# Optimization experiments

Measured on AMD Instinct MI355X. Metric: run time of the kernel, lower is better.

Reference implementation:

```python
import jax, jax.numpy as jnp
import numpy as np

B, L, C = 4, 8192, 256
HEADS = 1
DP = C // HEADS
FFN_HID = C * 2 * 4  # (d_model*2) * ffn_dim_expansion
EPS = 1e-5


def _layernorm(x, gamma, beta):
    mu = jnp.mean(x, axis=-1, keepdims=True)
    var = jnp.var(x, axis=-1, keepdims=True)
    return (x - mu) * jax.lax.rsqrt(var + EPS) * gamma + beta


def setup_inputs() -> dict:
    key = jax.random.key(0)
    ks = jax.random.split(key, 12)
    s = 0.02
    return {
        "source": jax.random.normal(ks[0], (B, L, C), jnp.float32),
        "target": jax.random.normal(ks[1], (B, L, C), jnp.float32),
        "Wq": jax.random.normal(ks[2], (C, C), jnp.float32) * s,
        "Wk": jax.random.normal(ks[3], (C, C), jnp.float32) * s,
        "Wv": jax.random.normal(ks[4], (C, C), jnp.float32) * s,
        "Wl": jax.random.normal(ks[5], (C, C), jnp.float32) * s,
        "gamma1": jnp.ones((C,), jnp.float32),
        "beta1": jnp.zeros((C,), jnp.float32),
        "W1": jax.random.normal(ks[6], (2 * C, FFN_HID), jnp.float32) * s,
        "b1": jnp.zeros((FFN_HID,), jnp.float32),
        "W2": jax.random.normal(ks[7], (FFN_HID, C), jnp.float32) * s,
        "b2": jnp.zeros((C,), jnp.float32),
        "gamma2": jnp.ones((C,), jnp.float32),
        "beta2": jnp.zeros((C,), jnp.float32),
        "h": 64,
        "w": 128,
    }


def reference(source, target, Wq, Wk, Wv, Wl, gamma1, beta1, W1, b1, W2, b2,
              gamma2, beta2, h, w):
    assert L == h * w
    q = (source @ Wq).reshape(B, L, HEADS, DP)
    k = (target @ Wk).reshape(B, L, HEADS, DP)
    v = (target @ Wv).reshape(B, L, HEADS, DP)
    k = jax.nn.softmax(k, axis=1)  # softmax over token dim
    context = jnp.einsum('bnhd,bnhe->bhde', q, k)   # small d×d per head
    attn = jnp.einsum('bhde,bnhe->bnhd', context, v).reshape(B, L, C)
    message = _layernorm(attn @ Wl, gamma1, beta1)
    hidden = jax.nn.gelu(jnp.concatenate([source, message], axis=-1) @ W1 + b1,
                         approximate=False)
    message = _layernorm(hidden @ W2 + b2, gamma2, beta2)
    return source + message
```

## Files before the change

### kernel.cpp

```cpp
#include <hip/hip_runtime.h>
#include <hip/hip_bf16.h>

typedef unsigned short u16;
typedef __attribute__((ext_vector_type(8))) short short8;
typedef __attribute__((ext_vector_type(4))) float f32x4;

#define B_    4
#define L_    8192
#define C_    256
#define BL_   (B_*L_)
#define BLC_  (BL_*C_)
#define FFN_  2048
#define KCAT_ 512
#define EPS_  1e-5f

__device__ __forceinline__ float bf2f(u16 v) {
  union { unsigned int u; float f; } x; x.u = ((unsigned int)v) << 16; return x.f;
}
__device__ __forceinline__ u16 f2bf(float f) {
  union { float f; unsigned int u; } x; x.f = f;
  unsigned int lsb = (x.u >> 16) & 1u;
  return (u16)((x.u + 0x7fffu + lsb) >> 16);
}
__device__ __forceinline__ float gelu_f(float x) {
  float z = fabsf(x) * 0.70710678118654752f;
  float t = __builtin_amdgcn_rcpf(1.f + 0.3275911f * z);
  float p = ((((1.061405429f * t - 1.453152027f) * t + 1.421413741f) * t
              - 0.284496736f) * t + 0.254829592f) * t;
  float e = __expf(-z * z);
  float erfv = copysignf(1.f - p * e, x);
  return 0.5f * x * (1.f + erfv);
}

template<int MODE, int ACT, int SPLITK>
__launch_bounds__(256, 2)
__global__ void gemm_abt(const u16* __restrict__ A0, const u16* __restrict__ A1,
                         int SEL, int lda,
                         const u16* __restrict__ Bt,
                         const float* __restrict__ bias,
                         u16* __restrict__ Cb, float* __restrict__ Cf,
                         int M, int N, int K,
                         long sAb, long sBb, long sCb)
{
  __shared__ __align__(16) u16 As[2 * 128 * 32];
  __shared__ __align__(16) u16 Bs[2 * 128 * 32];

  const int ntiles = N >> 7;
  const int tile = blockIdx.x;
  const int mt0 = (tile / ntiles) << 7;
  const int nt0 = (tile % ntiles) << 7;
  const int kchunk = K / (int)gridDim.y;
  const int k0beg = blockIdx.y * kchunk;
  const int k0end = k0beg + kchunk;
  const int bz = blockIdx.z;
  A0 += (long)bz * sAb;  A1 += (long)bz * sAb;  Bt += (long)bz * sBb;

  const u16* Abase = (MODE == 2 && nt0 >= SEL) ? A1 : A0;

  const int tid  = threadIdx.x;
  const int wave = tid >> 6, lane = tid & 63;
  const int srow = lane >> 2;
  const int cq   = lane & 3;
  const int gq   = cq ^ (srow & 3);
  const int frow = lane & 15;
  const int fq   = lane >> 4;
  const int fqx  = (fq ^ (frow & 3)) * 8;

  f32x4 zero = {0.f, 0.f, 0.f, 0.f};
  f32x4 acc[4][4];
#pragma unroll
  for (int i = 0; i < 4; i++)
#pragma unroll
    for (int j = 0; j < 4; j++) acc[i][j] = zero;

  const int wm = (wave & 1) * 64, wn = (wave >> 1) * 64;

  for (int k0 = k0beg; k0 < k0end; k0 += 64) {
    __syncthreads();
    const u16* Asrc;
    int ka;
    if (MODE == 1) {
      const bool lo = (k0 < SEL);
      Asrc = lo ? A0 : A1;
      ka = lo ? k0 : (k0 - SEL);
    } else { Asrc = Abase; ka = k0; }

#pragma unroll
    for (int h = 0; h < 2; h++) {
#pragma unroll
      for (int i = 0; i < 2; i++) {
        const int chunk = i * 4 + wave;
        const u16* ga = Asrc + (long)(mt0 + chunk * 16 + srow) * lda
                        + (ka + h * 32 + gq * 8);
        __builtin_amdgcn_global_load_lds(
            (const __attribute__((address_space(1))) unsigned int*)ga,
            (__attribute__((address_space(3))) unsigned int*)&As[h * 4096 + chunk * 16 * 32],
            16, 0, 0);
        const u16* gb = Bt + (long)(nt0 + chunk * 16 + srow) * K
                        + (k0 + h * 32 + gq * 8);
        __builtin_amdgcn_global_load_lds(
            (const __attribute__((address_space(1))) unsigned int*)gb,
            (__attribute__((address_space(3))) unsigned int*)&Bs[h * 4096 + chunk * 16 * 32],
            16, 0, 0);
      }
    }
    __syncthreads();

#pragma unroll
    for (int h = 0; h < 2; h++) {
      short8 af[4], bf[4];
#pragma unroll
      for (int t = 0; t < 4; t++)
        af[t] = *(const short8*)&As[h * 4096 + (wm + t * 16 + frow) * 32 + fqx];
#pragma unroll
      for (int t = 0; t < 4; t++)
        bf[t] = *(const short8*)&Bs[h * 4096 + (wn + t * 16 + frow) * 32 + fqx];
#pragma unroll
      for (int mt = 0; mt < 4; mt++)
#pragma unroll
        for (int nt = 0; nt < 4; nt++)
          acc[mt][nt] = __builtin_amdgcn_mfma_f32_16x16x32_bf16(af[mt], bf[nt], acc[mt][nt], 0, 0, 0);
    }
  }

  if (SPLITK) {
    float* Cp = Cf + (long)bz * sCb;
#pragma unroll
    for (int mt = 0; mt < 4; mt++)
#pragma unroll
      for (int r = 0; r < 4; r++) {
        const int row = mt0 + wm + mt * 16 + fq * 4 + r;
#pragma unroll
        for (int nt = 0; nt < 4; nt++) {
          const int col = nt0 + wn + nt * 16 + frow;
          atomicAdd(&Cp[(long)row * N + col], acc[mt][nt][r]);
        }
      }
  } else {
    u16* Cp = Cb + (long)bz * sCb;
    float bv[4];
#pragma unroll
    for (int nt = 0; nt < 4; nt++)
      bv[nt] = bias ? bias[nt0 + wn + nt * 16 + frow] : 0.f;
#pragma unroll
    for (int mt = 0; mt < 4; mt++)
#pragma unroll
      for (int r = 0; r < 4; r++) {
        const int row = mt0 + wm + mt * 16 + fq * 4 + r;
#pragma unroll
        for (int nt = 0; nt < 4; nt++) {
          const int col = nt0 + wn + nt * 16 + frow;
          float v = acc[mt][nt][r] + bv[nt];
          if (ACT == 1) v = gelu_f(v);
          Cp[(long)row * N + col] = f2bf(v);
        }
      }
  }
}

__global__ void transpose2d(const u16* __restrict__ in, u16* __restrict__ out,
                            int R, int Cc, int ldi, long sIb, long sOb)
{
  __shared__ u16 t[32][33];
  const int bx = blockIdx.x * 32;
  const int by = blockIdx.y * 32;
  in  += (long)blockIdx.z * sIb;
  out += (long)blockIdx.z * sOb;
  const int tx = threadIdx.x, ty = threadIdx.y;
#pragma unroll
  for (int i = ty; i < 32; i += 8)
    t[i][tx] = in[(long)(by + i) * ldi + bx + tx];
  __syncthreads();
#pragma unroll
  for (int i = ty; i < 32; i += 8)
    out[(long)(bx + i) * R + by + tx] = t[tx][i];
}

__global__ void transpose_f2b(const float* __restrict__ in, u16* __restrict__ out,
                              int R, int Cc)
{
  __shared__ u16 t[32][33];
  const int bx = blockIdx.x * 32;
  const int by = blockIdx.y * 32;
  const int tx = threadIdx.x, ty = threadIdx.y;
#pragma unroll
  for (int i = ty; i < 32; i += 8)
    t[i][tx] = f2bf(in[(long)(by + i) * Cc + bx + tx]);
  __syncthreads();
#pragma unroll
  for (int i = ty; i < 32; i += 8)
    out[(long)(bx + i) * R + by + tx] = t[tx][i];
}

__global__ void pack_w256(const float* __restrict__ w0, const float* __restrict__ w1,
                          const float* __restrict__ w2, const float* __restrict__ w3,
                          u16* __restrict__ qkvT, u16* __restrict__ wlT)
{
  __shared__ u16 t[32][33];
  const int z = blockIdx.z;
  const float* in = (z == 0) ? w0 : (z == 1) ? w1 : (z == 2) ? w2 : w3;
  u16* out = (z < 3) ? (qkvT + (long)z * C_ * C_) : wlT;
  const int bx = blockIdx.x * 32, by = blockIdx.y * 32;
  const int tx = threadIdx.x, ty = threadIdx.y;
#pragma unroll
  for (int i = ty; i < 32; i += 8)
    t[i][tx] = f2bf(in[(long)(by + i) * C_ + bx + tx]);
  __syncthreads();
#pragma unroll
  for (int i = ty; i < 32; i += 8)
    out[(long)(bx + i) * C_ + by + tx] = t[tx][i];
}

__global__ void cast2_f2b(const float* __restrict__ in0, const float* __restrict__ in1,
                          u16* __restrict__ out0, u16* __restrict__ out1)
{
  const float* in = blockIdx.y ? in1 : in0;
  u16* out = blockIdx.y ? out1 : out0;
  int i = (blockIdx.x * 256 + threadIdx.x) * 4;
  float4 v = *(const float4*)(in + i);
  ushort4 o; o.x = f2bf(v.x); o.y = f2bf(v.y); o.z = f2bf(v.z); o.w = f2bf(v.w);
  *(ushort4*)(out + i) = o;
}

__global__ void softmax_rows(u16* __restrict__ data, int rowlen)
{
  const long base = (long)blockIdx.x * rowlen;
  const int tid = threadIdx.x, wave = tid >> 6, lane = tid & 63;
  __shared__ float red[4];

  float m = -3.4e38f;
  for (int i = tid; i < rowlen; i += 256) m = fmaxf(m, bf2f(data[base + i]));
#pragma unroll
  for (int off = 32; off; off >>= 1) m = fmaxf(m, __shfl_xor(m, off, 64));
  if (lane == 0) red[wave] = m;
  __syncthreads();
  m = fmaxf(fmaxf(red[0], red[1]), fmaxf(red[2], red[3]));
  __syncthreads();

  float s = 0.f;
  for (int i = tid; i < rowlen; i += 256) s += expf(bf2f(data[base + i]) - m);
#pragma unroll
  for (int off = 32; off; off >>= 1) s += __shfl_xor(s, off, 64);
  if (lane == 0) red[wave] = s;
  __syncthreads();
  const float inv = 1.f / (red[0] + red[1] + red[2] + red[3]);
  for (int i = tid; i < rowlen; i += 256)
    data[base + i] = f2bf(expf(bf2f(data[base + i]) - m) * inv);
}

template<int OUTF>
__global__ void layernorm_rows(const u16* __restrict__ x,
                               const float* __restrict__ gamma,
                               const float* __restrict__ beta,
                               const float* __restrict__ src,
                               void* __restrict__ outv)
{
  const int wave = threadIdx.x >> 6, lane = threadIdx.x & 63;
  const long row = (long)blockIdx.x * 4 + wave;
  ushort4 raw = ((const ushort4*)(x + row * C_))[lane];
  float v0 = bf2f(raw.x), v1 = bf2f(raw.y), v2 = bf2f(raw.z), v3 = bf2f(raw.w);
  float s = v0 + v1 + v2 + v3;
  float q = v0 * v0 + v1 * v1 + v2 * v2 + v3 * v3;
#pragma unroll
  for (int off = 32; off; off >>= 1) {
    s += __shfl_xor(s, off, 64);
    q += __shfl_xor(q, off, 64);
  }
  const float mu  = s * (1.f / C_);
  const float var = q * (1.f / C_) - mu * mu;
  const float rs  = 1.f / sqrtf(var + EPS_);
  float4 gr = ((const float4*)gamma)[lane];
  float4 br = ((const float4*)beta)[lane];
  float o0 = (v0 - mu) * rs * gr.x + br.x;
  float o1 = (v1 - mu) * rs * gr.y + br.y;
  float o2 = (v2 - mu) * rs * gr.z + br.z;
  float o3 = (v3 - mu) * rs * gr.w + br.w;
  if (OUTF) {
    float4 sr = ((const float4*)(src + row * C_))[lane];
    float4 ow; ow.x = o0 + sr.x; ow.y = o1 + sr.y; ow.z = o2 + sr.z; ow.w = o3 + sr.w;
    ((float4*)((float*)outv + row * C_))[lane] = ow;
  } else {
    ushort4 ow; ow.x = f2bf(o0); ow.y = f2bf(o1); ow.z = f2bf(o2); ow.w = f2bf(o3);
    ((ushort4*)((u16*)outv + row * C_))[lane] = ow;
  }
}

__global__ void zero_f32(float* __restrict__ p, int n) {
  int i = blockIdx.x * 256 + threadIdx.x;
  if (i < n) p[i] = 0.f;
}
__global__ void f32_to_bf16_k(const float* __restrict__ in, u16* __restrict__ out, int n) {
  int i = blockIdx.x * 256 + threadIdx.x;
  if (i < n) out[i] = f2bf(in[i]);
}

extern "C" void kernel_launch(void* const* d_in, const int* in_sizes, int n_in,
                              void* d_out, int out_size, void* d_ws, size_t ws_size,
                              hipStream_t stream)
{
  const float* source = (const float*)d_in[0];
  const float* target = (const float*)d_in[1];
  const float* Wq     = (const float*)d_in[2];
  const float* Wk     = (const float*)d_in[3];
  const float* Wv     = (const float*)d_in[4];
  const float* Wl     = (const float*)d_in[5];
  const float* gamma1 = (const float*)d_in[6];
  const float* beta1  = (const float*)d_in[7];
  const float* W1     = (const float*)d_in[8];
  const float* b1     = (const float*)d_in[9];
  const float* W2     = (const float*)d_in[10];
  const float* b2     = (const float*)d_in[11];
  const float* gamma2 = (const float*)d_in[12];
  const float* beta2  = (const float*)d_in[13];
  (void)in_sizes; (void)n_in; (void)out_size;

  char* ws = (char*)d_ws;
  size_t off = 0;
  auto take = [&](size_t bytes) -> char* {
    char* p = ws + off; off += (bytes + 255) & ~(size_t)255; return p;
  };
  u16*   WqkvT = (u16*)take((size_t)768 * C_ * 2);
  u16*   WlT   = (u16*)take((size_t)C_ * C_ * 2);
  u16*   W1T   = (u16*)take((size_t)FFN_ * KCAT_ * 2);
  u16*   W2T   = (u16*)take((size_t)C_ * FFN_ * 2);
  float* ctxTf = (float*)take((size_t)B_ * C_ * C_ * 4);
  u16*   ctxTb = (u16*)take((size_t)B_ * C_ * C_ * 2);
  u16*   Mtb   = (u16*)take((size_t)B_ * C_ * C_ * 2);
  u16*   srcB  = (u16*)take((size_t)BLC_ * 2);
  u16*   bufB  = (u16*)take((size_t)BLC_ * 2);
  u16*   bufD  = (u16*)take((size_t)BLC_ * 2);
  u16*   bufE  = (u16*)take((size_t)BLC_ * 2);
  const size_t ubase = off;
  u16* tgtB = (u16*)(ws + ubase);
  u16* QKV  = (u16*)(ws + ubase + (size_t)BLC_ * 2);
  u16* qT   = (u16*)(ws + ubase + (size_t)BLC_ * 2 + (size_t)BL_ * 768 * 2);
  u16* kT   = qT + (size_t)BLC_;
  const size_t live = (size_t)BLC_ * 2 * 3 + (size_t)BL_ * 768 * 2;
  int nchunk = 1;
  while (nchunk < 16) {
    size_t hid = (size_t)(BL_ / nchunk) * FFN_ * 2;
    size_t need = ubase + (hid > live ? hid : live);
    if (need <= ws_size) break;
    nchunk <<= 1;
  }
  const int Mc = BL_ / nchunk;
  u16* hidden = (u16*)(ws + ubase);

  dim3 tb(32, 8);
  cast2_f2b<<<dim3(BLC_ / 1024, 2), 256, 0, stream>>>(source, target, srcB, tgtB);
  pack_w256<<<dim3(8, 8, 4), tb, 0, stream>>>(Wq, Wk, Wv, Wl, WqkvT, WlT);
  transpose_f2b<<<dim3(FFN_/32, KCAT_/32), tb, 0, stream>>>(W1, W1T, KCAT_, FFN_);
  transpose_f2b<<<dim3(C_/32,  FFN_/32), tb, 0, stream>>>(W2, W2T, FFN_, C_);
  zero_f32<<<(B_*C_*C_)/256, 256, 0, stream>>>(ctxTf, B_*C_*C_);

  gemm_abt<2,0,0><<<dim3((BL_/128)*(768/128)), 256, 0, stream>>>(
      srcB, tgtB, 256, C_, WqkvT, nullptr, QKV, nullptr, BL_, 768, C_, 0, 0, 0);

  transpose2d<<<dim3(C_/32, L_/32, B_), tb, 0, stream>>>(QKV,       qT, L_, C_, 768, (long)L_*768, (long)L_*C_);
  transpose2d<<<dim3(C_/32, L_/32, B_), tb, 0, stream>>>(QKV + 256, kT, L_, C_, 768, (long)L_*768, (long)L_*C_);
  softmax_rows<<<B_*C_, 256, 0, stream>>>(kT, L_);

  gemm_abt<0,0,1><<<dim3(4, 16, B_), 256, 0, stream>>>(
      kT, kT, 0, L_, qT, nullptr, nullptr, ctxTf, C_, C_, L_,
      (long)C_*L_, (long)C_*L_, (long)C_*C_);
  f32_to_bf16_k<<<(B_*C_*C_)/256, 256, 0, stream>>>(ctxTf, ctxTb, B_*C_*C_);

  gemm_abt<0,0,0><<<dim3(4, 1, B_), 256, 0, stream>>>(
      WlT, WlT, 0, C_, ctxTb, nullptr, Mtb, nullptr, C_, C_, C_,
      0, (long)C_*C_, (long)C_*C_);

  gemm_abt<0,0,0><<<dim3((L_/128)*(C_/128), 1, B_), 256, 0, stream>>>(
      QKV + 512, QKV + 512, 0, 768, Mtb, nullptr, bufB, nullptr, L_, C_, C_,
      (long)L_*768, (long)C_*C_, (long)L_*C_);

  layernorm_rows<0><<<BL_/4, 256, 0, stream>>>(bufB, gamma1, beta1, nullptr, bufD);

  for (int ch = 0; ch < nchunk; ch++) {
    const long moff = (long)ch * Mc;
    gemm_abt<1,1,0><<<dim3((Mc/128)*(FFN_/128)), 256, 0, stream>>>(
        srcB + moff * C_, bufD + moff * C_, C_, C_, W1T, b1, hidden, nullptr,
        Mc, FFN_, KCAT_, 0, 0, 0);
    gemm_abt<0,0,0><<<dim3((Mc/128)*(C_/128)), 256, 0, stream>>>(
        hidden, hidden, 0, FFN_, W2T, b2, bufE + moff * C_, nullptr,
        Mc, C_, FFN_, 0, 0, 0);
  }

  layernorm_rows<1><<<BL_/4, 256, 0, stream>>>(bufE, gamma2, beta2, source, d_out);
}
```

Measured before the change: 420.3 us.

## Fuse LayerNorms into GEMM epilogues and fold Wl into Wq to reassociate attention

Adds a gemm_ln kernel whose 64x256 tile covers full rows, so both LayerNorms run in the GEMM epilogue and the separate layernorm passes and intermediate buffers go away. It precomputes Wq·Wl so the context matrix is built directly as (q·Wl)^T k in fp32. That fp32 matrix is converted to bf16 inside the V GEMM, which removes the ctx-to-bf16 conversion and the extra small GEMM. Weight packing, input casting and zeroing, and the Q/K transposes are merged into fewer launches. Tile ordering is switched to M-major. In exchange there are larger per-block tiles with occupancy risk, an extra rounding from folding Wl into Wq in bf16, and uncoalesced fp32 B loads in the fused kernel.

```diff
diff --git a/kernel.cpp b/kernel.cpp
--- a/kernel.cpp
+++ b/kernel.cpp
@@ -11,8 +11,11 @@
 #define BL_   (B_*L_)
 #define BLC_  (BL_*C_)
 #define FFN_  2048
-#define KCAT_ 512
 #define EPS_  1e-5f
+
+#define GLDS(dst, src) __builtin_amdgcn_global_load_lds( \
+    (const __attribute__((address_space(1))) unsigned int*)(src), \
+    (__attribute__((address_space(3))) unsigned int*)(dst), 16, 0, 0)
 
 __device__ __forceinline__ float bf2f(u16 v) {
   union { unsigned int u; float f; } x; x.u = ((unsigned int)v) << 16; return x.f;
@@ -45,10 +48,10 @@
   __shared__ __align__(16) u16 As[2 * 128 * 32];
   __shared__ __align__(16) u16 Bs[2 * 128 * 32];
 
-  const int ntiles = N >> 7;
+  const int mtiles = M >> 7;
   const int tile = blockIdx.x;
-  const int mt0 = (tile / ntiles) << 7;
-  const int nt0 = (tile % ntiles) << 7;
+  const int mt0 = (tile % mtiles) << 7;
+  const int nt0 = (tile / mtiles) << 7;
   const int kchunk = K / (int)gridDim.y;
   const int k0beg = blockIdx.y * kchunk;
   const int k0end = k0beg + kchunk;
@@ -60,8 +63,7 @@
   const int tid  = threadIdx.x;
   const int wave = tid >> 6, lane = tid & 63;
   const int srow = lane >> 2;
-  const int cq   = lane & 3;
-  const int gq   = cq ^ (srow & 3);
+  const int gq   = (lane & 3) ^ (srow & 3);
   const int frow = lane & 15;
   const int fq   = lane >> 4;
   const int fqx  = (fq ^ (frow & 3)) * 8;
@@ -84,28 +86,18 @@
       Asrc = lo ? A0 : A1;
       ka = lo ? k0 : (k0 - SEL);
     } else { Asrc = Abase; ka = k0; }
-
 #pragma unroll
     for (int h = 0; h < 2; h++) {
 #pragma unroll
       for (int i = 0; i < 2; i++) {
         const int chunk = i * 4 + wave;
-        const u16* ga = Asrc + (long)(mt0 + chunk * 16 + srow) * lda
-                        + (ka + h * 32 + gq * 8);
-        __builtin_amdgcn_global_load_lds(
-            (const __attribute__((address_space(1))) unsigned int*)ga,
-            (__attribute__((address_space(3))) unsigned int*)&As[h * 4096 + chunk * 16 * 32],
-            16, 0, 0);
-        const u16* gb = Bt + (long)(nt0 + chunk * 16 + srow) * K
-                        + (k0 + h * 32 + gq * 8);
-        __builtin_amdgcn_global_load_lds(
-            (const __attribute__((address_space(1))) unsigned int*)gb,
-            (__attribute__((address_space(3))) unsigned int*)&Bs[h * 4096 + chunk * 16 * 32],
-            16, 0, 0);
+        GLDS(&As[h * 4096 + chunk * 512],
+             Asrc + (long)(mt0 + chunk * 16 + srow) * lda + (ka + h * 32 + gq * 8));
+        GLDS(&Bs[h * 4096 + chunk * 512],
+             Bt + (long)(nt0 + chunk * 16 + srow) * K + (k0 + h * 32 + gq * 8));
       }
     }
     __syncthreads();
-
 #pragma unroll
     for (int h = 0; h < 2; h++) {
       short8 af[4], bf[4];
@@ -131,10 +123,8 @@
       for (int r = 0; r < 4; r++) {
         const int row = mt0 + wm + mt * 16 + fq * 4 + r;
 #pragma unroll
-        for (int nt = 0; nt < 4; nt++) {
-          const int col = nt0 + wn + nt * 16 + frow;
-          atomicAdd(&Cp[(long)row * N + col], acc[mt][nt][r]);
-        }
+        for (int nt = 0; nt < 4; nt++)
+          atomicAdd(&Cp[(long)row * N + nt0 + wn + nt * 16 + frow], acc[mt][nt][r]);
       }
   } else {
     u16* Cp = Cb + (long)bz * sCb;
@@ -149,77 +139,214 @@
         const int row = mt0 + wm + mt * 16 + fq * 4 + r;
 #pragma unroll
         for (int nt = 0; nt < 4; nt++) {
-          const int col = nt0 + wn + nt * 16 + frow;
           float v = acc[mt][nt][r] + bv[nt];
           if (ACT == 1) v = gelu_f(v);
-          Cp[(long)row * N + col] = f2bf(v);
+          Cp[(long)row * N + nt0 + wn + nt * 16 + frow] = f2bf(v);
         }
       }
   }
 }
 
-__global__ void transpose2d(const u16* __restrict__ in, u16* __restrict__ out,
-                            int R, int Cc, int ldi, long sIb, long sOb)
+template<int CVTB, int OUTF>
+__launch_bounds__(256, 3)
+__global__ void gemm_ln(const u16* __restrict__ A, long sAb, int lda, int K,
+                        const void* __restrict__ Btv, long sBb, int zshift,
+                        const float* __restrict__ bias,
+                        const float* __restrict__ gamma, const float* __restrict__ beta,
+                        const float* __restrict__ src, void* __restrict__ outv,
+                        long Moff)
+{
+  __shared__ __align__(16) u16 As[2 * 64 * 32];
+  __shared__ __align__(16) u16 Bs[2 * 256 * 32];
+  __shared__ float red_s[64][4], red_q[64][4];
+
+  const int gm0 = blockIdx.x * 64;
+  const int z = gm0 >> zshift;
+  const int ml = gm0 - (z << zshift);
+  A += (long)z * sAb + (long)ml * lda;
+  const float* Bf = (const float*)Btv + (CVTB ? (long)z * sBb : 0);
+  const u16*   Bb = (const u16*)Btv   + (CVTB ? 0 : (long)z * sBb);
+
+  const int tid = threadIdx.x, wave = tid >> 6, lane = tid & 63;
+  const int srow = lane >> 2, gq = (lane & 3) ^ (srow & 3);
+  const int frow = lane & 15, fq = lane >> 4;
+  const int fqx = (fq ^ (frow & 3)) * 8;
+  const int wn = wave * 64;
+
+  f32x4 zero = {0.f, 0.f, 0.f, 0.f};
+  f32x4 acc[4][4];
+#pragma unroll
+  for (int i = 0; i < 4; i++)
+#pragma unroll
+    for (int j = 0; j < 4; j++) acc[i][j] = zero;
+
+  for (int k0 = 0; k0 < K; k0 += 64) {
+    __syncthreads();
+#pragma unroll
+    for (int h = 0; h < 2; h++) {
+      GLDS(&As[h * 2048 + wave * 512],
+           A + (long)(wave * 16 + srow) * lda + (k0 + h * 32 + gq * 8));
+#pragma unroll
+      for (int i = 0; i < 4; i++) {
+        const int chunk = i * 4 + wave;
+        if (CVTB) {
+          const float* bp = Bf + (long)(chunk * 16 + srow) * K + (k0 + h * 32 + gq * 8);
+          float4 p0 = *(const float4*)bp;
+          float4 p1 = *(const float4*)(bp + 4);
+          short8 w;
+          w[0] = (short)f2bf(p0.x); w[1] = (short)f2bf(p0.y);
+          w[2] = (short)f2bf(p0.z); w[3] = (short)f2bf(p0.w);
+          w[4] = (short)f2bf(p1.x); w[5] = (short)f2bf(p1.y);
+          w[6] = (short)f2bf(p1.z); w[7] = (short)f2bf(p1.w);
+          *(short8*)&Bs[h * 8192 + chunk * 512 + srow * 32 + (lane & 3) * 8] = w;
+        } else {
+          GLDS(&Bs[h * 8192 + chunk * 512],
+               Bb + (long)(chunk * 16 + srow) * K + (k0 + h * 32 + gq * 8));
+        }
+      }
+    }
+    __syncthreads();
+#pragma unroll
+    for (int h = 0; h < 2; h++) {
+      short8 af[4], bf[4];
+#pragma unroll
+      for (int t = 0; t < 4; t++)
+        af[t] = *(const short8*)&As[h * 2048 + (t * 16 + frow) * 32 + fqx];
+#pragma unroll
+      for (int t = 0; t < 4; t++)
+        bf[t] = *(const short8*)&Bs[h * 8192 + (wn + t * 16 + frow) * 32 + fqx];
+#pragma unroll
+      for (int mt = 0; mt < 4; mt++)
+#pragma unroll
+        for (int nt = 0; nt < 4; nt++)
+          acc[mt][nt] = __builtin_amdgcn_mfma_f32_16x16x32_bf16(af[mt], bf[nt], acc[mt][nt], 0, 0, 0);
+    }
+  }
+
+  float gv[4], bv[4], b2v[4];
+#pragma unroll
+  for (int nt = 0; nt < 4; nt++) {
+    const int col = wn + nt * 16 + frow;
+    gv[nt] = gamma[col]; bv[nt] = beta[col];
+    b2v[nt] = OUTF ? bias[col] : 0.f;
+  }
+#pragma unroll
+  for (int mt = 0; mt < 4; mt++)
+#pragma unroll
+    for (int r = 0; r < 4; r++) {
+      float s = 0.f, q = 0.f;
+#pragma unroll
+      for (int nt = 0; nt < 4; nt++) {
+        float v = acc[mt][nt][r] + b2v[nt];
+        acc[mt][nt][r] = v; s += v; q += v * v;
+      }
+#pragma unroll
+      for (int m = 1; m < 16; m <<= 1) {
+        s += __shfl_xor(s, m, 16); q += __shfl_xor(q, m, 16);
+      }
+      if (frow == 0) {
+        const int row = mt * 16 + fq * 4 + r;
+        red_s[row][wave] = s; red_q[row][wave] = q;
+      }
+    }
+  __syncthreads();
+#pragma unroll
+  for (int mt = 0; mt < 4; mt++)
+#pragma unroll
+    for (int r = 0; r < 4; r++) {
+      const int row = mt * 16 + fq * 4 + r;
+      float4 ss = *(const float4*)red_s[row];
+      float4 qq = *(const float4*)red_q[row];
+      const float s = ss.x + ss.y + ss.z + ss.w;
+      const float q = qq.x + qq.y + qq.z + qq.w;
+      const float mu = s * (1.f / 256.f);
+      const float var = q * (1.f / 256.f) - mu * mu;
+      const float rs = 1.f / sqrtf(var + EPS_);
+      const long grow = Moff + gm0 + row;
+#pragma unroll
+      for (int nt = 0; nt < 4; nt++) {
+        const int col = wn + nt * 16 + frow;
+        const float o = (acc[mt][nt][r] - mu) * rs * gv[nt] + bv[nt];
+        if (OUTF)
+          ((float*)outv)[grow * 256 + col] = o + src[grow * 256 + col];
+        else
+          ((u16*)outv)[grow * 256 + col] = f2bf(o);
+      }
+    }
+}
+
+__global__ void weightpack(const float* __restrict__ Wq, const float* __restrict__ Wk,
+                           const float* __restrict__ Wv, const float* __restrict__ Wl,
+                           const float* __restrict__ W1, const float* __restrict__ W2,
+                           u16* __restrict__ WqC, u16* __restrict__ WlT,
+                           u16* __restrict__ WqkvT, u16* __restrict__ W1T,
+                           u16* __restrict__ W2T)
 {
   __shared__ u16 t[32][33];
-  const int bx = blockIdx.x * 32;
-  const int by = blockIdx.y * 32;
-  in  += (long)blockIdx.z * sIb;
-  out += (long)blockIdx.z * sOb;
-  const int tx = threadIdx.x, ty = threadIdx.y;
+  const int bid = blockIdx.x, tx = threadIdx.x, ty = threadIdx.y;
+  const float* in; u16* out; int Cc, R, bx, by;
+  if (bid < 256) {
+    const int w = bid >> 6, tt = bid & 63;
+    bx = (tt & 7) * 32; by = (tt >> 3) * 32; Cc = 256; R = 256;
+    if (w == 0) {
+#pragma unroll
+      for (int i = ty; i < 32; i += 8)
+        WqC[(long)(by + i) * 256 + bx + tx] = f2bf(Wq[(long)(by + i) * 256 + bx + tx]);
+      return;
+    }
+    in  = (w == 1) ? Wl : (w == 2) ? Wk : Wv;
+    out = (w == 1) ? WlT : (w == 2) ? (WqkvT + 65536) : (WqkvT + 131072);
+  } else if (bid < 1280) {
+    const int l = bid - 256; bx = (l & 63) * 32; by = (l >> 6) * 32;
+    in = W1; out = W1T; Cc = 2048; R = 512;
+  } else {
+    const int l = bid - 1280; bx = (l & 7) * 32; by = (l >> 3) * 32;
+    in = W2; out = W2T; Cc = 256; R = 2048;
+  }
 #pragma unroll
   for (int i = ty; i < 32; i += 8)
-    t[i][tx] = in[(long)(by + i) * ldi + bx + tx];
+    t[i][tx] = f2bf(in[(long)(by + i) * Cc + bx + tx]);
   __syncthreads();
 #pragma unroll
   for (int i = ty; i < 32; i += 8)
     out[(long)(bx + i) * R + by + tx] = t[tx][i];
 }
 
-__global__ void transpose_f2b(const float* __restrict__ in, u16* __restrict__ out,
-                              int R, int Cc)
+__global__ void castzero(const float* __restrict__ src, const float* __restrict__ tgt,
+                         u16* __restrict__ srcB, u16* __restrict__ tgtB,
+                         float* __restrict__ Mtf)
+{
+  const int x = blockIdx.x;
+  if (x < BLC_ / 1024) {
+    const float* in = blockIdx.y ? tgt : src;
+    u16* out = blockIdx.y ? tgtB : srcB;
+    const int i = (x * 256 + threadIdx.x) * 4;
+    float4 v = *(const float4*)(in + i);
+    ushort4 o; o.x = f2bf(v.x); o.y = f2bf(v.y); o.z = f2bf(v.z); o.w = f2bf(v.w);
+    *(ushort4*)(out + i) = o;
+  } else if (blockIdx.y == 0) {
+    const int i = ((x - BLC_ / 1024) * 256 + threadIdx.x) * 4;
+    float4 zv = {0.f, 0.f, 0.f, 0.f};
+    *(float4*)(Mtf + i) = zv;
+  }
+}
+
+__global__ void transQK(const u16* __restrict__ QKV,
+                        u16* __restrict__ qlT, u16* __restrict__ kT)
 {
   __shared__ u16 t[32][33];
-  const int bx = blockIdx.x * 32;
-  const int by = blockIdx.y * 32;
-  const int tx = threadIdx.x, ty = threadIdx.y;
-#pragma unroll
-  for (int i = ty; i < 32; i += 8)
-    t[i][tx] = f2bf(in[(long)(by + i) * Cc + bx + tx]);
-  __syncthreads();
-#pragma unroll
-  for (int i = ty; i < 32; i += 8)
-    out[(long)(bx + i) * R + by + tx] = t[tx][i];
-}
-
-__global__ void pack_w256(const float* __restrict__ w0, const float* __restrict__ w1,
-                          const float* __restrict__ w2, const float* __restrict__ w3,
-                          u16* __restrict__ qkvT, u16* __restrict__ wlT)
-{
-  __shared__ u16 t[32][33];
-  const int z = blockIdx.z;
-  const float* in = (z == 0) ? w0 : (z == 1) ? w1 : (z == 2) ? w2 : w3;
-  u16* out = (z < 3) ? (qkvT + (long)z * C_ * C_) : wlT;
+  const int z = blockIdx.z, zb = z & 3;
+  const u16* in = QKV + (long)zb * L_ * 768 + (z < 4 ? 0 : 256);
+  u16* out = (z < 4 ? qlT : kT) + (long)zb * L_ * C_;
   const int bx = blockIdx.x * 32, by = blockIdx.y * 32;
   const int tx = threadIdx.x, ty = threadIdx.y;
 #pragma unroll
   for (int i = ty; i < 32; i += 8)
-    t[i][tx] = f2bf(in[(long)(by + i) * C_ + bx + tx]);
+    t[i][tx] = in[(long)(by + i) * 768 + bx + tx];
   __syncthreads();
 #pragma unroll
   for (int i = ty; i < 32; i += 8)
-    out[(long)(bx + i) * C_ + by + tx] = t[tx][i];
-}
-
-__global__ void cast2_f2b(const float* __restrict__ in0, const float* __restrict__ in1,
-                          u16* __restrict__ out0, u16* __restrict__ out1)
-{
-  const float* in = blockIdx.y ? in1 : in0;
-  u16* out = blockIdx.y ? out1 : out0;
-  int i = (blockIdx.x * 256 + threadIdx.x) * 4;
-  float4 v = *(const float4*)(in + i);
-  ushort4 o; o.x = f2bf(v.x); o.y = f2bf(v.y); o.z = f2bf(v.z); o.w = f2bf(v.w);
-  *(ushort4*)(out + i) = o;
+    out[(long)(bx + i) * L_ + by + tx] = t[tx][i];
 }
 
 __global__ void softmax_rows(u16* __restrict__ data, int rowlen)
@@ -246,52 +373,6 @@
   const float inv = 1.f / (red[0] + red[1] + red[2] + red[3]);
   for (int i = tid; i < rowlen; i += 256)
     data[base + i] = f2bf(expf(bf2f(data[base + i]) - m) * inv);
-}
-
-template<int OUTF>
-__global__ void layernorm_rows(const u16* __restrict__ x,
-                               const float* __restrict__ gamma,
-                               const float* __restrict__ beta,
-                               const float* __restrict__ src,
-                               void* __restrict__ outv)
-{
-  const int wave = threadIdx.x >> 6, lane = threadIdx.x & 63;
-  const long row = (long)blockIdx.x * 4 + wave;
-  ushort4 raw = ((const ushort4*)(x + row * C_))[lane];
-  float v0 = bf2f(raw.x), v1 = bf2f(raw.y), v2 = bf2f(raw.z), v3 = bf2f(raw.w);
-  float s = v0 + v1 + v2 + v3;
-  float q = v0 * v0 + v1 * v1 + v2 * v2 + v3 * v3;
-#pragma unroll
-  for (int off = 32; off; off >>= 1) {
-    s += __shfl_xor(s, off, 64);
-    q += __shfl_xor(q, off, 64);
-  }
-  const float mu  = s * (1.f / C_);
-  const float var = q * (1.f / C_) - mu * mu;
-  const float rs  = 1.f / sqrtf(var + EPS_);
-  float4 gr = ((const float4*)gamma)[lane];
-  float4 br = ((const float4*)beta)[lane];
-  float o0 = (v0 - mu) * rs * gr.x + br.x;
-  float o1 = (v1 - mu) * rs * gr.y + br.y;
-  float o2 = (v2 - mu) * rs * gr.z + br.z;
-  float o3 = (v3 - mu) * rs * gr.w + br.w;
-  if (OUTF) {
-    float4 sr = ((const float4*)(src + row * C_))[lane];
-    float4 ow; ow.x = o0 + sr.x; ow.y = o1 + sr.y; ow.z = o2 + sr.z; ow.w = o3 + sr.w;
-    ((float4*)((float*)outv + row * C_))[lane] = ow;
-  } else {
-    ushort4 ow; ow.x = f2bf(o0); ow.y = f2bf(o1); ow.z = f2bf(o2); ow.w = f2bf(o3);
-    ((ushort4*)((u16*)outv + row * C_))[lane] = ow;
-  }
-}
-
-__global__ void zero_f32(float* __restrict__ p, int n) {
-  int i = blockIdx.x * 256 + threadIdx.x;
-  if (i < n) p[i] = 0.f;
-}
-__global__ void f32_to_bf16_k(const float* __restrict__ in, u16* __restrict__ out, int n) {
-  int i = blockIdx.x * 256 + threadIdx.x;
-  if (i < n) out[i] = f2bf(in[i]);
 }
 
 extern "C" void kernel_launch(void* const* d_in, const int* in_sizes, int n_in,
@@ -320,70 +401,58 @@
     char* p = ws + off; off += (bytes + 255) & ~(size_t)255; return p;
   };
   u16*   WqkvT = (u16*)take((size_t)768 * C_ * 2);
+  u16*   WqC   = (u16*)take((size_t)C_ * C_ * 2);
   u16*   WlT   = (u16*)take((size_t)C_ * C_ * 2);
-  u16*   W1T   = (u16*)take((size_t)FFN_ * KCAT_ * 2);
+  u16*   W1T   = (u16*)take((size_t)FFN_ * 512 * 2);
   u16*   W2T   = (u16*)take((size_t)C_ * FFN_ * 2);
-  float* ctxTf = (float*)take((size_t)B_ * C_ * C_ * 4);
-  u16*   ctxTb = (u16*)take((size_t)B_ * C_ * C_ * 2);
-  u16*   Mtb   = (u16*)take((size_t)B_ * C_ * C_ * 2);
+  float* Mtf   = (float*)take((size_t)B_ * C_ * C_ * 4);
   u16*   srcB  = (u16*)take((size_t)BLC_ * 2);
-  u16*   bufB  = (u16*)take((size_t)BLC_ * 2);
-  u16*   bufD  = (u16*)take((size_t)BLC_ * 2);
-  u16*   bufE  = (u16*)take((size_t)BLC_ * 2);
+  u16*   msg   = (u16*)take((size_t)BLC_ * 2);
   const size_t ubase = off;
-  u16* tgtB = (u16*)(ws + ubase);
-  u16* QKV  = (u16*)(ws + ubase + (size_t)BLC_ * 2);
-  u16* qT   = (u16*)(ws + ubase + (size_t)BLC_ * 2 + (size_t)BL_ * 768 * 2);
-  u16* kT   = qT + (size_t)BLC_;
-  const size_t live = (size_t)BLC_ * 2 * 3 + (size_t)BL_ * 768 * 2;
+  u16*   tgtB  = (u16*)take((size_t)BLC_ * 2);
+  u16*   QKV   = (u16*)take((size_t)BL_ * 768 * 2);
+  u16*   qlT   = (u16*)take((size_t)BLC_ * 2);
+  u16*   kT    = (u16*)take((size_t)BLC_ * 2);
+  const size_t pool = off - ubase;
+  u16*   hidden = (u16*)(ws + ubase);
+
   int nchunk = 1;
-  while (nchunk < 16) {
-    size_t hid = (size_t)(BL_ / nchunk) * FFN_ * 2;
-    size_t need = ubase + (hid > live ? hid : live);
+  for (; nchunk < 8; nchunk <<= 1) {
+    size_t hid = ((size_t)BL_ / nchunk) * FFN_ * 2;
+    size_t need = ubase + (hid > pool ? hid : pool);
     if (need <= ws_size) break;
-    nchunk <<= 1;
   }
   const int Mc = BL_ / nchunk;
-  u16* hidden = (u16*)(ws + ubase);
 
   dim3 tb(32, 8);
-  cast2_f2b<<<dim3(BLC_ / 1024, 2), 256, 0, stream>>>(source, target, srcB, tgtB);
-  pack_w256<<<dim3(8, 8, 4), tb, 0, stream>>>(Wq, Wk, Wv, Wl, WqkvT, WlT);
-  transpose_f2b<<<dim3(FFN_/32, KCAT_/32), tb, 0, stream>>>(W1, W1T, KCAT_, FFN_);
-  transpose_f2b<<<dim3(C_/32,  FFN_/32), tb, 0, stream>>>(W2, W2T, FFN_, C_);
-  zero_f32<<<(B_*C_*C_)/256, 256, 0, stream>>>(ctxTf, B_*C_*C_);
-
-  gemm_abt<2,0,0><<<dim3((BL_/128)*(768/128)), 256, 0, stream>>>(
+  weightpack<<<1792, tb, 0, stream>>>(Wq, Wk, Wv, Wl, W1, W2, WqC, WlT, WqkvT, W1T, W2T);
+  castzero<<<dim3(BLC_ / 1024 + (B_ * C_ * C_) / 1024, 2), 256, 0, stream>>>(
+      source, target, srcB, tgtB, Mtf);
+
+  gemm_abt<0,0,0><<<4, 256, 0, stream>>>(
+      WlT, WlT, 0, C_, WqC, nullptr, WqkvT, nullptr, C_, C_, C_, 0, 0, 0);
+
+  gemm_abt<2,0,0><<<(BL_/128)*(768/128), 256, 0, stream>>>(
       srcB, tgtB, 256, C_, WqkvT, nullptr, QKV, nullptr, BL_, 768, C_, 0, 0, 0);
 
-  transpose2d<<<dim3(C_/32, L_/32, B_), tb, 0, stream>>>(QKV,       qT, L_, C_, 768, (long)L_*768, (long)L_*C_);
-  transpose2d<<<dim3(C_/32, L_/32, B_), tb, 0, stream>>>(QKV + 256, kT, L_, C_, 768, (long)L_*768, (long)L_*C_);
+  transQK<<<dim3(8, L_/32, 8), tb, 0, stream>>>(QKV, qlT, kT);
   softmax_rows<<<B_*C_, 256, 0, stream>>>(kT, L_);
 
   gemm_abt<0,0,1><<<dim3(4, 16, B_), 256, 0, stream>>>(
-      kT, kT, 0, L_, qT, nullptr, nullptr, ctxTf, C_, C_, L_,
+      qlT, qlT, 0, L_, kT, nullptr, nullptr, Mtf, C_, C_, L_,
       (long)C_*L_, (long)C_*L_, (long)C_*C_);
-  f32_to_bf16_k<<<(B_*C_*C_)/256, 256, 0, stream>>>(ctxTf, ctxTb, B_*C_*C_);
-
-  gemm_abt<0,0,0><<<dim3(4, 1, B_), 256, 0, stream>>>(
-      WlT, WlT, 0, C_, ctxTb, nullptr, Mtb, nullptr, C_, C_, C_,
-      0, (long)C_*C_, (long)C_*C_);
-
-  gemm_abt<0,0,0><<<dim3((L_/128)*(C_/128), 1, B_), 256, 0, stream>>>(
-      QKV + 512, QKV + 512, 0, 768, Mtb, nullptr, bufB, nullptr, L_, C_, C_,
-      (long)L_*768, (long)C_*C_, (long)L_*C_);
-
-  layernorm_rows<0><<<BL_/4, 256, 0, stream>>>(bufB, gamma1, beta1, nullptr, bufD);
+
+  gemm_ln<1,0><<<BL_/64, 256, 0, stream>>>(
+      QKV + 512, (long)L_*768, 768, 256, Mtf, (long)C_*C_, 13,
+      nullptr, gamma1, beta1, nullptr, msg, 0);
 
   for (int ch = 0; ch < nchunk; ch++) {
     const long moff = (long)ch * Mc;
-    gemm_abt<1,1,0><<<dim3((Mc/128)*(FFN_/128)), 256, 0, stream>>>(
-        srcB + moff * C_, bufD + moff * C_, C_, C_, W1T, b1, hidden, nullptr,
-        Mc, FFN_, KCAT_, 0, 0, 0);
-    gemm_abt<0,0,0><<<dim3((Mc/128)*(C_/128)), 256, 0, stream>>>(
-        hidden, hidden, 0, FFN_, W2T, b2, bufE + moff * C_, nullptr,
-        Mc, C_, FFN_, 0, 0, 0);
-  }
-
-  layernorm_rows<1><<<BL_/4, 256, 0, stream>>>(bufE, gamma2, beta2, source, d_out);
-}
+    gemm_abt<1,1,0><<<(Mc/128)*(FFN_/128), 256, 0, stream>>>(
+        srcB + moff * C_, msg + moff * C_, 256, C_, W1T, b1, hidden, nullptr,
+        Mc, FFN_, 512, 0, 0, 0);
+    gemm_ln<0,1><<<Mc/64, 256, 0, stream>>>(
+        hidden, 0, FFN_, FFN_, W2T, 0, 30,
+        b2, gamma2, beta2, source, d_out, moff);
+  }
+}
```

Measured after the change: 419.3 us. Within noise of the previous version (-0.2%).
